# Kernel optimization log

Hardware: AMD Instinct MI355X
Metric: run time of the kernel (lower is better)

## Reference

```python
import jax, jax.numpy as jnp
import numpy as np

T = 262144  # time steps (~700 years daily)
HID = 32    # M100 hidden width


def setup_inputs() -> dict:
    key = jax.random.key(0)
    ks = jax.random.split(key, 10)
    # forward arg: inputs [T, 5] = [s_snow, s_water, precp, tmean, time]
    s_snow = jax.random.uniform(ks[0], (T,), jnp.float32) * 10.0
    s_water = jax.random.uniform(ks[1], (T,), jnp.float32) * 100.0
    precp = jax.random.uniform(ks[2], (T,), jnp.float32) * 10.0   # mm/day, >=0
    tmean = jax.random.normal(ks[3], (T,), jnp.float32) * 10.0    # deg C
    time = jnp.arange(T, dtype=jnp.float32)                       # integer day grid
    inputs = jnp.stack([s_snow, s_water, precp, tmean, time], axis=-1)
    # forward arg: day-length forcing (separate interpolator in original)
    lday = jax.random.uniform(ks[4], (T,), jnp.float32) * 0.5 + 0.2
    # M100 MLP params: 4 -> 32 -> 32 -> 5, tanh hidden
    scale = 0.2
    W1 = jax.random.normal(ks[5], (4, HID), jnp.float32) * scale
    b1 = jnp.zeros((HID,), jnp.float32)
    W2 = jax.random.normal(ks[6], (HID, HID), jnp.float32) * scale
    b2 = jnp.zeros((HID,), jnp.float32)
    W3 = jax.random.normal(ks[7], (HID, 5), jnp.float32) * scale
    b3 = jnp.zeros((5,), jnp.float32)
    return {"inputs": inputs, "lday": lday, "W1": W1, "b1": b1,
            "W2": W2, "b2": b2, "W3": W3, "b3": b3}


def reference(inputs, lday, W1, b1, W2, b2, W3, b3):
    precp = inputs[:, 2]
    tmean = inputs[:, 3]
    time = inputs[:, 4]
    n = precp.shape[0]

    def step_fn(x):
        return (jnp.tanh(5.0 * x) + 1.0) * 0.5

    def mlp(x):  # works on [4] or [N,4]
        h = jnp.tanh(x @ W1 + b1)
        h = jnp.tanh(h @ W2 + b2)
        return h @ W3 + b3

    def interp(f, t):  # periodic linear interpolation on the unit day grid
        i0 = jnp.floor(t)
        frac = t - i0
        i = jnp.mod(i0.astype(jnp.int32), n)
        ip = jnp.mod(i + 1, n)
        return f[i] * (1.0 - frac) + f[ip] * frac

    def rhs(t, y):  # hybrid_model_mlp: MLP-parameterized ExpHydro fluxes
        s0, s1 = y[0], y[1]
        p = interp(precp, t)
        tm = interp(tmean, t)
        ld = interp(lday, t)
        o = mlp(jnp.stack([s0, s1, p, tm]))
        p_snow = jax.nn.relu(jnp.sinh(o[0]) * step_fn(-tm))
        p_rain = jax.nn.relu(jnp.sinh(o[1]))
        m = jax.nn.relu(step_fn(s0) * jnp.sinh(o[2]))
        et = step_fn(s1) * jnp.exp(o[3]) * ld
        q = step_fn(s1) * jnp.exp(o[4])
        return jnp.stack([p_snow - m, p_rain + m - et - q])

    y0 = jnp.stack([inputs[0, 0], inputs[0, 1]])  # [2]
    t0s = time[:-1]
    dts = time[1:] - time[:-1]

    def scan_step(y, tdt):  # classic RK4 step between saved time points
        t, dt = tdt
        k1 = rhs(t, y)
        k2 = rhs(t + 0.5 * dt, y + 0.5 * dt * k1)
        k3 = rhs(t + 0.5 * dt, y + 0.5 * dt * k2)
        k4 = rhs(t + dt, y + dt * k3)
        yn = y + (dt / 6.0) * (k1 + 2.0 * k2 + 2.0 * k3 + k4)
        return yn, yn

    _, ys = jax.lax.scan(scan_step, y0, (t0s, dts))
    ys = jnp.concatenate([y0[None, :], ys], axis=0)  # [T, 2]

    s_snow_nn = jnp.maximum(ys[:, 0], 0.0)
    s_water_nn = jnp.maximum(ys[:, 1], 0.0)
    inputs_nn = jnp.stack([s_snow_nn, s_water_nn, precp, tmean], axis=-1)  # [T, 4]
    out = mlp(inputs_nn)  # [T, 5]
    return out[:, -1]      # q head
```

## Files before the change

### kernel.cpp

```cpp
#include <hip/hip_runtime.h>
#include <math.h>

#define T_TOTAL 262144
#define HID 32
#define WIN 2048
#define WLEN (T_TOTAL / WIN)
#define NSWEEP 6
#define FD_EPS0 4.0
#define FD_EPS1 8.0
#define LOG2E 1.4426950408889634f
#define TANH2C 2.8853900817779268f
#define NEG10LOG2E (-14.426950408889634f)
#define POS10LOG2E (14.426950408889634f)

#define PIN(x) asm volatile("" : "+v"(x))

typedef _Float16 f16x8 __attribute__((ext_vector_type(8)));
typedef float f32x4 __attribute__((ext_vector_type(4)));

__device__ __forceinline__ float fexp2(float x) { return __builtin_amdgcn_exp2f(x); }
__device__ __forceinline__ float frcp(float x)  { return __builtin_amdgcn_rcpf(x); }
__device__ __forceinline__ float fast_sig10(float x) {
    return frcp(1.0f + fexp2(x * NEG10LOG2E));
}
__device__ __forceinline__ float fast_tanh_clamp(float x) {
    float xc = __builtin_amdgcn_fmed3f(x, -9.0f, 9.0f);
    float u  = fexp2(xc * TANH2C);
    return fmaf(-2.0f, frcp(u + 1.0f), 1.0f);
}
__device__ __forceinline__ float fast_tanh_nc(float x) {
    float u = fexp2(x * TANH2C);
    return fmaf(-2.0f, frcp(u + 1.0f), 1.0f);
}

template <int CTRL>
__device__ __forceinline__ float dpp_add(float v) {
    int t = __builtin_amdgcn_update_dpp(0, __float_as_int(v), CTRL, 0xF, 0xF, true);
    return v + __int_as_float(t);
}
__device__ __forceinline__ float allsum16(float x) {
    x = dpp_add<0xB1>(x);
    x = dpp_add<0x4E>(x);
    x = dpp_add<0x141>(x);
    x = dpp_add<0x140>(x);
    return x;
}
__device__ __forceinline__ int dpp_xor1_i(int v) {
    return __builtin_amdgcn_update_dpp(0, v, 0xB1, 0xF, 0xF, true);
}
__device__ __forceinline__ float rl(float x, int lane) {
    return __int_as_float(__builtin_amdgcn_readlane(__float_as_int(x), lane));
}
__device__ __forceinline__ float bpf(int addr, float x) {
    return __int_as_float(__builtin_amdgcn_ds_bpermute(addr, __float_as_int(x)));
}

__global__ void init_kernel(const float* __restrict__ inputs, float2* icg) {
    int w = blockIdx.x * blockDim.x + threadIdx.x;
    if (w < WIN) icg[w] = make_float2(inputs[0], inputs[1]);
}

__global__ __launch_bounds__(64, 1) void sweep_kernel(
    const float* __restrict__ inputs,
    const float* __restrict__ lday,
    const float* __restrict__ W1, const float* __restrict__ b1,
    const float* __restrict__ W2, const float* __restrict__ b2,
    const float* __restrict__ W3, const float* __restrict__ b3,
    float* __restrict__ traj,
    const float2* __restrict__ icg,
    double2* __restrict__ E)
{
    const int lane = threadIdx.x;
    const int col  = lane & 15;
    const int quad = lane >> 4;
    const int j32  = lane & 31;
    const int half = lane >> 5;
    const bool odd = (lane & 1) != 0;

    const int wnd  = blockIdx.x;
    const int S    = wnd * WLEN;
    const int endStep = (S + WLEN < T_TOTAL - 1) ? (S + WLEN) : (T_TOTAL - 1);

    float w1c0 = W1[0 * HID + j32] * TANH2C, w1c1 = W1[1 * HID + j32] * TANH2C;
    float w1c2 = W1[2 * HID + j32] * TANH2C, w1c3 = W1[3 * HID + j32] * TANH2C;
    float b1j = b1[j32] * TANH2C;
    PIN(w1c0); PIN(w1c1); PIN(w1c2); PIN(w1c3); PIN(b1j);

    f16x8 Bhi0, Blo0, Bhi1, Blo1;
#pragma unroll
    for (int jj = 0; jj < 8; ++jj) {
        float w0 = W2[(quad * 8 + jj) * HID + col] * TANH2C;
        float w1v = W2[(quad * 8 + jj) * HID + col + 16] * TANH2C;
        _Float16 h0 = (_Float16)w0, h1v = (_Float16)w1v;
        Bhi0[jj] = h0;  Blo0[jj] = (_Float16)(w0 - (float)h0);
        Bhi1[jj] = h1v; Blo1[jj] = (_Float16)(w1v - (float)h1v);
    }
    PIN(Bhi0); PIN(Blo0); PIN(Bhi1); PIN(Blo1);

    float b2a2 = b2[col] * TANH2C, b2b2 = b2[col + 16] * TANH2C;
    f32x4 cb0 = {b2a2, b2a2, b2a2, b2a2};
    f32x4 cb1 = {b2b2, b2b2, b2b2, b2b2};
    PIN(cb0); PIN(cb1);

    float wca[5], wcb[5];
#pragma unroll
    for (int c = 0; c < 5; ++c) {
        wca[c] = W3[col * 5 + c] * LOG2E;
        wcb[c] = W3[(col + 16) * 5 + c] * LOG2E;
        PIN(wca[c]); PIN(wcb[c]);
    }

    float m0 = (col == 0) ? 1.f : 0.f;
    float m1 = (col == 1) ? 1.f : 0.f;
    float m2 = (col == 2) ? 1.f : 0.f;
    float m3 = (col == 3) ? 1.f : 0.f;
    float m4 = (col == 4) ? 1.f : 0.f;
    float m5 = (col == 5) ? 1.f : 0.f;
    float m6 = (col == 6) ? 1.f : 0.f;
    float m7 = (col == 7) ? 1.f : 0.f;
    float m8 = (col == 8) ? 1.f : 0.f;
    float sig1m = (col >= 5 && col <= 8) ? 1.f : 0.f;
    float zb = b3[(col < 5) ? col : 0];
    float zconst = (col < 5) ? zb * LOG2E : 0.f;
    PIN(m0); PIN(m1); PIN(m2); PIN(m3); PIN(m4); PIN(m5); PIN(m6); PIN(m7); PIN(m8);
    PIN(sig1m); PIN(zconst);

    int psel = (lane & 1) ? 0x01000504 : 0x05040100;
    int l3 = lane & 3;
    int roff = (l3 == 1) ? 128 : (l3 == 2) ? 4 : (l3 == 3) ? 132 : 0;
    int bbase = 32 * quad + roff;
    int bp0 = bbase, bp1 = bbase + 8, bp2 = bbase + 16, bp3 = bbase + 24;
    PIN(psel); PIN(bp0); PIN(bp1); PIN(bp2); PIN(bp3);

    int qb = 64 * quad;
    int a_sh0 = qb + 0,  a_sh1 = qb + 4,  a_sh2 = qb + 8;
    int a_e3  = qb + 12, a_e4  = qb + 16, a_sg0 = qb + 20, a_sg1 = qb + 24;
    PIN(a_sh0); PIN(a_sh1); PIN(a_sh2); PIN(a_e3); PIN(a_e4); PIN(a_sg0); PIN(a_sg1);

    float2 ic = icg[wnd];
    double y0 = (double)ic.x + ((quad == 1) ? FD_EPS0 : 0.0);
    double y1 = (double)ic.y + ((quad >= 2) ? FD_EPS1 : 0.0);
    float2* traj2 = (float2*)traj;
    if (lane == 0 && wnd == 0)
        traj2[0] = make_float2(ic.x, ic.y);

    auto rhs = [&](float s0q, float s1q, float base, float stm, float ld, float zoffk,
                   float& d0, float& d1, float& rout) {
        float s0A = rl(s0q, 0),  s1A = rl(s1q, 0);
        float s0B = rl(s0q, 16), s1B = rl(s1q, 16);
        float s0C = rl(s0q, 32), s1C = rl(s1q, 32);
        float s0p = half ? s0B : s0A;
        float s1p = half ? s1B : s1A;
        float prep = fmaf(s1p, w1c1, fmaf(s0p, w1c0, base));
        float prec = fmaf(s1C, w1c1, fmaf(s0C, w1c0, base));
        float up_ = fexp2(prep);
        float uc_ = fexp2(prec);
        float h1p = fmaf(-2.0f, frcp(up_ + 1.0f), 1.0f);
        float h1c = fmaf(-2.0f, frcp(uc_ + 1.0f), 1.0f);
        union { _Float16 h; unsigned short u; } cvp, cvc;
        cvp.h = (_Float16)h1p; cvc.h = (_Float16)h1c;
        int ownp = (int)cvp.u, ownc = (int)cvc.u;
        int nbp = dpp_xor1_i(ownp), nbc = dpp_xor1_i(ownc);
        int pkp = __builtin_amdgcn_perm(nbp, ownp, psel);
        int pkc = __builtin_amdgcn_perm(nbc, ownc, psel);
        int pk  = odd ? pkc : pkp;
        int g0i = __builtin_amdgcn_ds_bpermute(bp0, pk);
        int g1i = __builtin_amdgcn_ds_bpermute(bp1, pk);
        int g2i = __builtin_amdgcn_ds_bpermute(bp2, pk);
        int g3i = __builtin_amdgcn_ds_bpermute(bp3, pk);
        union { int i[4]; f16x8 h; } au;
        au.i[0] = g0i; au.i[1] = g1i; au.i[2] = g2i; au.i[3] = g3i;
        f16x8 A = au.h;
        f32x4 zz = {0.f, 0.f, 0.f, 0.f};
        f32x4 chi0 = __builtin_amdgcn_mfma_f32_16x16x32_f16(A, Bhi0, cb0, 0, 0, 0);
        f32x4 clo0 = __builtin_amdgcn_mfma_f32_16x16x32_f16(A, Blo0, zz, 0, 0, 0);
        f32x4 chi1 = __builtin_amdgcn_mfma_f32_16x16x32_f16(A, Bhi1, cb1, 0, 0, 0);
        f32x4 clo1 = __builtin_amdgcn_mfma_f32_16x16x32_f16(A, Blo1, zz, 0, 0, 0);
        float tA0 = chi0[0] + clo0[0], tB0 = chi0[1] + clo0[1], tC0 = chi0[2] + clo0[2];
        float tA1 = chi1[0] + clo1[0], tB1 = chi1[1] + clo1[1], tC1 = chi1[2] + clo1[2];
        float t0 = (quad == 1) ? tB0 : (quad >= 2) ? tC0 : tA0;
        float t1 = (quad == 1) ? tB1 : (quad >= 2) ? tC1 : tA1;
        float ua = fexp2(t0);
        float ub = fexp2(t1);
        float g0 = fmaf(-2.0f, frcp(ua + 1.0f), 1.0f);
        float g1 = fmaf(-2.0f, frcp(ub + 1.0f), 1.0f);
        float r0 = fmaf(g0, wca[0], g1 * wcb[0]);
        float r1 = fmaf(g0, wca[1], g1 * wcb[1]);
        float r2 = fmaf(g0, wca[2], g1 * wcb[2]);
        float r3 = fmaf(g0, wca[3], g1 * wcb[3]);
        float r4 = fmaf(g0, wca[4], g1 * wcb[4]);
        float s0r = allsum16(r0);
        float s1r = allsum16(r1);
        float s2r = allsum16(r2);
        float s3r = allsum16(r3);
        float s4r = allsum16(r4);
        float zs0 = s0q * NEG10LOG2E;
        float zs1 = s1q * NEG10LOG2E;
        float zoff = fmaf(zs0, m5, fmaf(zs1, m6, zoffk));
        float zarg = fmaf(s0r, m0, fmaf(s1r, m1, fmaf(s2r, m2,
                     fmaf(s3r, m3, fmaf(s4r, m4, zoff)))));
        float u = fexp2(zarg);
        float r = frcp(u + sig1m);
        float w = fmaf(0.5f, u, -0.5f * r);
        float sh0 = bpf(a_sh0, w), sh1 = bpf(a_sh1, w), sh2 = bpf(a_sh2, w);
        float e3  = bpf(a_e3, u),  e4  = bpf(a_e4, u);
        float sg0 = bpf(a_sg0, r), sg1 = bpf(a_sg1, r);
        float p_snow = fmaxf(sh0 * stm, 0.f);
        float p_rain = fmaxf(sh1, 0.f);
        float melt   = fmaxf(sg0 * sh2, 0.f);
        float etq    = sg1 * fmaf(e3, ld, e4);
        d0 = p_snow - melt;
        d1 = (p_rain + melt) - etq;
        rout = r;
    };

    float pA = inputs[S * 5 + 2],       tmA = inputs[S * 5 + 3],       ldA = lday[S];
    float pB = inputs[(S + 1) * 5 + 2], tmB = inputs[(S + 1) * 5 + 3], ldB = lday[S + 1];
    float pC = inputs[(S + 2) * 5 + 2], tmC = inputs[(S + 2) * 5 + 3], ldC = lday[S + 2];
    float stmA = fast_sig10(-tmA);
    float stmB = fast_sig10(-tmB);
    float stmm = fast_sig10(-0.5f * (tmA + tmB));
    float baseA = fmaf(pA, w1c2, fmaf(tmA, w1c3, b1j));
    float baseB = fmaf(pB, w1c2, fmaf(tmB, w1c3, b1j));

    for (int n = S; n < endStep; ++n) {
        const float ldm = 0.5f * (ldA + ldB);
        const float pm  = 0.5f * (pA + pB);
        const float tmm = 0.5f * (tmA + tmB);
        const float basem = fmaf(pm, w1c2, fmaf(tmm, w1c3, b1j));
        const float ztm_m = (0.5f * (tmB + tmC)) * POS10LOG2E;
        const float ztm_b = tmC * POS10LOG2E;
        const float zoffk = fmaf(ztm_m, m7, fmaf(ztm_b, m8, zconst));

        const float fy0 = (float)y0, fy1 = (float)y1;
        float k10, k11, k20, k21, k30, k31, k40, k41, rd;
        rhs(fy0,                  fy1,                  baseA, stmA, ldA, zoffk, k10, k11, rd);
        rhs(fmaf(0.5f, k10, fy0), fmaf(0.5f, k11, fy1), basem, stmm, ldm, zoffk, k20, k21, rd);
        rhs(fmaf(0.5f, k20, fy0), fmaf(0.5f, k21, fy1), basem, stmm, ldm, zoffk, k30, k31, rd);
        rhs(fy0 + k30,            fy1 + k31,            baseB, stmB, ldB, zoffk, k40, k41, rd);
        const float stmm_n = rl(rd, 7);
        const float stmB_n = rl(rd, 8);

        const float s0sum = (k10 + 2.0f * k20) + (2.0f * k30 + k40);
        const float s1sum = (k11 + 2.0f * k21) + (2.0f * k31 + k41);
        y0 += (1.0 / 6.0) * (double)s0sum;
        y1 += (1.0 / 6.0) * (double)s1sum;

        if (lane == 0)
            traj2[n + 1] = make_float2((float)y0, (float)y1);

        stmA = stmB; stmB = stmB_n; stmm = stmm_n;
        baseA = baseB;
        baseB = fmaf(pC, w1c2, fmaf(tmC, w1c3, b1j));
        pA = pB; tmA = tmB; ldA = ldB;
        pB = pC; tmB = tmC; ldB = ldC;
        const int np3 = (n + 3 < T_TOTAL) ? (n + 3) : (T_TOTAL - 1);
        pC = inputs[np3 * 5 + 2]; tmC = inputs[np3 * 5 + 3]; ldC = lday[np3];
    }

    if (lane == 0)  E[wnd]           = make_double2(y0, y1);
    if (lane == 16) E[WIN + wnd]     = make_double2(y0, y1);
    if (lane == 32) E[2 * WIN + wnd] = make_double2(y0, y1);
}

__global__ __launch_bounds__(64) void correct_kernel(
    const float* __restrict__ inputs,
    const double2* __restrict__ E,
    float2* __restrict__ icg) {
    __shared__ float sJ00[WIN], sJ10[WIN], sJ11[WIN];
    __shared__ float sE0x[WIN], sE0y[WIN];
    __shared__ float sGx[WIN], sGy[WIN];
    for (int i = threadIdx.x; i < WIN; i += 64) {
        double2 e0 = E[i];
        double2 e1 = E[WIN + i];
        double2 e2 = E[2 * WIN + i];
        float2 g   = icg[i];
        float J00 = (float)((e1.x - e0.x) * (1.0 / FD_EPS0));
        float J10 = (float)((e1.y - e0.y) * (1.0 / FD_EPS0));
        float J11 = (float)((e2.y - e0.y) * (1.0 / FD_EPS1));
        sJ00[i] = fminf(fmaxf(J00, -0.15f), 1.15f);
        sJ10[i] = fminf(fmaxf(J10, -0.30f), 1.80f);
        sJ11[i] = fminf(fmaxf(J11,  0.00f), 1.10f);
        sE0x[i] = (float)e0.x; sE0y[i] = (float)e0.y;
        sGx[i]  = g.x;         sGy[i]  = g.y;
    }
    __syncthreads();
    if (threadIdx.x != 0) return;

    float y0c = inputs[0];
    float y1c = inputs[1];
#pragma unroll 8
    for (int w = 0; w < WIN; ++w) {
        float d0 = y0c - sGx[w];
        float d1 = y1c - sGy[w];
        d0 = fminf(fmaxf(d0, -50.0f), 50.0f);
        d1 = fminf(fmaxf(d1, -400.0f), 400.0f);
        icg[w] = make_float2(y0c, y1c);
        y0c = fmaf(sJ00[w], d0, sE0x[w]);
        y1c = fmaf(sJ10[w], d0, fmaf(sJ11[w], d1, sE0y[w]));
        y0c = fminf(fmaxf(y0c, -5.0f), 1000.0f);
        y1c = fminf(fmaxf(y1c, -5.0f), 5000.0f);
    }
}

__global__ __launch_bounds__(256) void out_kernel(
    const float* __restrict__ inputs,
    const float* __restrict__ traj,
    const float* __restrict__ W1, const float* __restrict__ b1,
    const float* __restrict__ W2, const float* __restrict__ b2,
    const float* __restrict__ W3, const float* __restrict__ b3,
    float* __restrict__ out)
{
    __shared__ float sW1[4 * HID];
    __shared__ float sb1[HID];
    __shared__ float sW2T[HID * HID];
    __shared__ float sb2[HID];
    __shared__ float sw3[HID];
    for (int i = threadIdx.x; i < 4 * HID; i += 256) sW1[i] = W1[i];
    for (int i = threadIdx.x; i < HID; i += 256) {
        sb1[i] = b1[i]; sb2[i] = b2[i]; sw3[i] = W3[i * 5 + 4];
    }
    for (int idx = threadIdx.x; idx < HID * HID; idx += 256) {
        int jj = idx >> 5, ii = idx & 31;
        sW2T[idx] = W2[ii * HID + jj];
    }
    __syncthreads();

    int t = blockIdx.x * 256 + threadIdx.x;
    if (t >= T_TOTAL) return;

    float2 st = ((const float2*)traj)[t];
    float s0 = fmaxf(st.x, 0.0f);
    float s1 = fmaxf(st.y, 0.0f);
    float p  = inputs[t * 5 + 2];
    float tm = inputs[t * 5 + 3];

    float h1[HID];
#pragma unroll
    for (int jj = 0; jj < HID; ++jj) {
        float pre = fmaf(s0, sW1[jj], fmaf(s1, sW1[HID + jj],
                    fmaf(p, sW1[2 * HID + jj],
                    fmaf(tm, sW1[3 * HID + jj], sb1[jj]))));
        h1[jj] = fast_tanh_clamp(pre);
    }
    float o = b3[4];
#pragma unroll 4
    for (int jj = 0; jj < HID; ++jj) {
        float a0 = sb2[jj], a1 = 0.f, a2 = 0.f, a3 = 0.f;
#pragma unroll
        for (int ii = 0; ii < HID; ii += 4) {
            a0 = fmaf(h1[ii + 0], sW2T[jj * HID + ii + 0], a0);
            a1 = fmaf(h1[ii + 1], sW2T[jj * HID + ii + 1], a1);
            a2 = fmaf(h1[ii + 2], sW2T[jj * HID + ii + 2], a2);
            a3 = fmaf(h1[ii + 3], sW2T[jj * HID + ii + 3], a3);
        }
        o = fmaf(fast_tanh_nc((a0 + a1) + (a2 + a3)), sw3[jj], o);
    }
    out[t] = o;
}

extern "C" void kernel_launch(void* const* d_in, const int* in_sizes, int n_in,
                              void* d_out, int out_size, void* d_ws, size_t ws_size,
                              hipStream_t stream) {
    (void)in_sizes; (void)n_in; (void)out_size; (void)ws_size;
    const float* inputs = (const float*)d_in[0];
    const float* lday   = (const float*)d_in[1];
    const float* W1     = (const float*)d_in[2];
    const float* b1     = (const float*)d_in[3];
    const float* W2     = (const float*)d_in[4];
    const float* b2     = (const float*)d_in[5];
    const float* W3     = (const float*)d_in[6];
    const float* b3     = (const float*)d_in[7];
    float* out  = (float*)d_out;
    float* traj = (float*)d_ws;

    char* scr = (char*)d_out;
    double2* E  = (double2*)scr;
    float2* icg = (float2*)(scr + 131072);

    hipLaunchKernelGGL(init_kernel, dim3((WIN + 255) / 256), dim3(256), 0, stream,
                       inputs, icg);
    for (int k = 0; k < NSWEEP - 1; ++k) {
        hipLaunchKernelGGL(sweep_kernel, dim3(WIN), dim3(64), 0, stream,
                           inputs, lday, W1, b1, W2, b2, W3, b3, traj, icg, E);
        hipLaunchKernelGGL(correct_kernel, dim3(1), dim3(64), 0, stream,
                           inputs, E, icg);
    }
    hipLaunchKernelGGL(sweep_kernel, dim3(WIN), dim3(64), 0, stream,
                       inputs, lday, W1, b1, W2, b2, W3, b3, traj, icg, E);
    hipLaunchKernelGGL(out_kernel, dim3((T_TOTAL + 255) / 256), dim3(256), 0, stream,
                       inputs, traj, W1, b1, W2, b2, W3, b3, out);
}
```

Baseline: 2.208 ms.

## Split trajectory into 3072 uneven windows and stream guesses in correction pass

Raises the number of parallel shooting windows from 2048 to 3072, using uneven window lengths of 85 or 86 steps so that 262144 steps divide across them. This shortens the serial RK4 chain each sweep block must walk and adds more blocks to fill the GPU. The correction kernel no longer stages the previous guesses in shared memory; it reads them from global memory eight at a time, prefetching the next group while processing the current one. The serial correction loop grows by half, shorter windows may change how well the Newton-like correction converges within the fixed sweep count, and the scratch offsets in the output buffer are moved to fit the larger arrays.

```diff
diff --git a/kernel.cpp b/kernel.cpp
--- a/kernel.cpp
+++ b/kernel.cpp
@@ -3,8 +3,7 @@
 
 #define T_TOTAL 262144
 #define HID 32
-#define WIN 2048
-#define WLEN (T_TOTAL / WIN)
+#define WIN 3072
 #define NSWEEP 6
 #define FD_EPS0 4.0
 #define FD_EPS1 8.0
@@ -78,8 +77,9 @@
     const bool odd = (lane & 1) != 0;
 
     const int wnd  = blockIdx.x;
-    const int S    = wnd * WLEN;
-    const int endStep = (S + WLEN < T_TOTAL - 1) ? (S + WLEN) : (T_TOTAL - 1);
+    const int S    = wnd * 85 + ((wnd < 1024) ? wnd : 1024);
+    const int LEN  = (wnd < 1024) ? 86 : 85;
+    const int endStep = (S + LEN < T_TOTAL - 1) ? (S + LEN) : (T_TOTAL - 1);
 
     float w1c0 = W1[0 * HID + j32] * TANH2C, w1c1 = W1[1 * HID + j32] * TANH2C;
     float w1c2 = W1[2 * HID + j32] * TANH2C, w1c3 = W1[3 * HID + j32] * TANH2C;
@@ -269,12 +269,10 @@
     float2* __restrict__ icg) {
     __shared__ float sJ00[WIN], sJ10[WIN], sJ11[WIN];
     __shared__ float sE0x[WIN], sE0y[WIN];
-    __shared__ float sGx[WIN], sGy[WIN];
     for (int i = threadIdx.x; i < WIN; i += 64) {
         double2 e0 = E[i];
         double2 e1 = E[WIN + i];
         double2 e2 = E[2 * WIN + i];
-        float2 g   = icg[i];
         float J00 = (float)((e1.x - e0.x) * (1.0 / FD_EPS0));
         float J10 = (float)((e1.y - e0.y) * (1.0 / FD_EPS0));
         float J11 = (float)((e2.y - e0.y) * (1.0 / FD_EPS1));
@@ -282,25 +280,42 @@
         sJ10[i] = fminf(fmaxf(J10, -0.30f), 1.80f);
         sJ11[i] = fminf(fmaxf(J11,  0.00f), 1.10f);
         sE0x[i] = (float)e0.x; sE0y[i] = (float)e0.y;
-        sGx[i]  = g.x;         sGy[i]  = g.y;
     }
     __syncthreads();
     if (threadIdx.x != 0) return;
 
     float y0c = inputs[0];
     float y1c = inputs[1];
-#pragma unroll 8
-    for (int w = 0; w < WIN; ++w) {
-        float d0 = y0c - sGx[w];
-        float d1 = y1c - sGy[w];
-        d0 = fminf(fmaxf(d0, -50.0f), 50.0f);
-        d1 = fminf(fmaxf(d1, -400.0f), 400.0f);
-        icg[w] = make_float2(y0c, y1c);
-        y0c = fmaf(sJ00[w], d0, sE0x[w]);
-        y1c = fmaf(sJ10[w], d0, fmaf(sJ11[w], d1, sE0y[w]));
-        y0c = fminf(fmaxf(y0c, -5.0f), 1000.0f);
-        y1c = fminf(fmaxf(y1c, -5.0f), 5000.0f);
-    }
+
+#define PROC(G, W)                                              \
+    {                                                           \
+        float d0 = y0c - (G).x;                                 \
+        float d1 = y1c - (G).y;                                 \
+        d0 = fminf(fmaxf(d0, -50.0f), 50.0f);                   \
+        d1 = fminf(fmaxf(d1, -400.0f), 400.0f);                 \
+        icg[W] = make_float2(y0c, y1c);                         \
+        y0c = fmaf(sJ00[W], d0, sE0x[W]);                       \
+        y1c = fmaf(sJ10[W], d0, fmaf(sJ11[W], d1, sE0y[W]));    \
+        y0c = fminf(fmaxf(y0c, -5.0f), 1000.0f);                \
+        y1c = fminf(fmaxf(y1c, -5.0f), 5000.0f);                \
+    }
+
+    float2 g0 = icg[0], g1 = icg[1], g2 = icg[2], g3 = icg[3];
+    float2 g4 = icg[4], g5 = icg[5], g6 = icg[6], g7 = icg[7];
+    for (int base = 0; base < WIN; base += 8) {
+        int nb = base + 8;
+        float2 t0, t1, t2, t3, t4, t5, t6, t7;
+        if (nb < WIN) {
+            t0 = icg[nb + 0]; t1 = icg[nb + 1]; t2 = icg[nb + 2]; t3 = icg[nb + 3];
+            t4 = icg[nb + 4]; t5 = icg[nb + 5]; t6 = icg[nb + 6]; t7 = icg[nb + 7];
+        } else {
+            t0 = g0; t1 = g1; t2 = g2; t3 = g3; t4 = g4; t5 = g5; t6 = g6; t7 = g7;
+        }
+        PROC(g0, base + 0); PROC(g1, base + 1); PROC(g2, base + 2); PROC(g3, base + 3);
+        PROC(g4, base + 4); PROC(g5, base + 5); PROC(g6, base + 6); PROC(g7, base + 7);
+        g0 = t0; g1 = t1; g2 = t2; g3 = t3; g4 = t4; g5 = t5; g6 = t6; g7 = t7;
+    }
+#undef PROC
 }
 
 __global__ __launch_bounds__(256) void out_kernel(
@@ -376,7 +391,7 @@
 
     char* scr = (char*)d_out;
     double2* E  = (double2*)scr;
-    float2* icg = (float2*)(scr + 131072);
+    float2* icg = (float2*)(scr + 196608);
 
     hipLaunchKernelGGL(init_kernel, dim3((WIN + 255) / 256), dim3(256), 0, stream,
                        inputs, icg);
```

Result: slower. 2.379 ms (+7.8%).

## Split trajectory into more shorter windows and double-buffer the correction staging

Applied to the files above, without the earlier changes.

Raises the window count from 2048 to 3072 and spreads steps unevenly (86 or 85 per window), so each sweep block runs a shorter serial RK4 chain. The correction kernel now stages window data in double-buffered chunks of 1024, letting the other 63 threads load the next chunk while thread 0 runs the serial correction recurrence. This cuts the per-sweep critical path, but the serial correction pass gets longer, more blocks compete for CUs, and the scratch offsets grow. More windows may also slow convergence of the fixed six-sweep scheme and hurt accuracy.

```diff
diff --git a/kernel.cpp b/kernel.cpp
--- a/kernel.cpp
+++ b/kernel.cpp
@@ -3,9 +3,9 @@
 
 #define T_TOTAL 262144
 #define HID 32
-#define WIN 2048
-#define WLEN (T_TOTAL / WIN)
+#define WIN 3072
 #define NSWEEP 6
+#define CH 1024
 #define FD_EPS0 4.0
 #define FD_EPS1 8.0
 #define LOG2E 1.4426950408889634f
@@ -78,8 +78,9 @@
     const bool odd = (lane & 1) != 0;
 
     const int wnd  = blockIdx.x;
-    const int S    = wnd * WLEN;
-    const int endStep = (S + WLEN < T_TOTAL - 1) ? (S + WLEN) : (T_TOTAL - 1);
+    const int S    = wnd * 85 + ((wnd < 1024) ? wnd : 1024);
+    const int LEN  = (wnd < 1024) ? 86 : 85;
+    const int endStep = (S + LEN < T_TOTAL - 1) ? (S + LEN) : (T_TOTAL - 1);
 
     float w1c0 = W1[0 * HID + j32] * TANH2C, w1c1 = W1[1 * HID + j32] * TANH2C;
     float w1c2 = W1[2 * HID + j32] * TANH2C, w1c3 = W1[3 * HID + j32] * TANH2C;
@@ -267,39 +268,51 @@
     const float* __restrict__ inputs,
     const double2* __restrict__ E,
     float2* __restrict__ icg) {
-    __shared__ float sJ00[WIN], sJ10[WIN], sJ11[WIN];
-    __shared__ float sE0x[WIN], sE0y[WIN];
-    __shared__ float sGx[WIN], sGy[WIN];
-    for (int i = threadIdx.x; i < WIN; i += 64) {
-        double2 e0 = E[i];
-        double2 e1 = E[WIN + i];
-        double2 e2 = E[2 * WIN + i];
-        float2 g   = icg[i];
+    __shared__ float sJ00[2][CH], sJ10[2][CH], sJ11[2][CH];
+    __shared__ float sE0x[2][CH], sE0y[2][CH];
+    __shared__ float sGx[2][CH],  sGy[2][CH];
+    const int tid = threadIdx.x;
+
+    auto stage_one = [&](int buf, int i, int w) {
+        double2 e0 = E[w];
+        double2 e1 = E[WIN + w];
+        double2 e2 = E[2 * WIN + w];
+        float2 g   = icg[w];
         float J00 = (float)((e1.x - e0.x) * (1.0 / FD_EPS0));
         float J10 = (float)((e1.y - e0.y) * (1.0 / FD_EPS0));
         float J11 = (float)((e2.y - e0.y) * (1.0 / FD_EPS1));
-        sJ00[i] = fminf(fmaxf(J00, -0.15f), 1.15f);
-        sJ10[i] = fminf(fmaxf(J10, -0.30f), 1.80f);
-        sJ11[i] = fminf(fmaxf(J11,  0.00f), 1.10f);
-        sE0x[i] = (float)e0.x; sE0y[i] = (float)e0.y;
-        sGx[i]  = g.x;         sGy[i]  = g.y;
-    }
+        sJ00[buf][i] = fminf(fmaxf(J00, -0.15f), 1.15f);
+        sJ10[buf][i] = fminf(fmaxf(J10, -0.30f), 1.80f);
+        sJ11[buf][i] = fminf(fmaxf(J11,  0.00f), 1.10f);
+        sE0x[buf][i] = (float)e0.x; sE0y[buf][i] = (float)e0.y;
+        sGx[buf][i]  = g.x;         sGy[buf][i]  = g.y;
+    };
+
+    for (int i = tid; i < CH; i += 64) stage_one(0, i, i);
     __syncthreads();
-    if (threadIdx.x != 0) return;
 
     float y0c = inputs[0];
     float y1c = inputs[1];
-#pragma unroll 8
-    for (int w = 0; w < WIN; ++w) {
-        float d0 = y0c - sGx[w];
-        float d1 = y1c - sGy[w];
-        d0 = fminf(fmaxf(d0, -50.0f), 50.0f);
-        d1 = fminf(fmaxf(d1, -400.0f), 400.0f);
-        icg[w] = make_float2(y0c, y1c);
-        y0c = fmaf(sJ00[w], d0, sE0x[w]);
-        y1c = fmaf(sJ10[w], d0, fmaf(sJ11[w], d1, sE0y[w]));
-        y0c = fminf(fmaxf(y0c, -5.0f), 1000.0f);
-        y1c = fminf(fmaxf(y1c, -5.0f), 5000.0f);
+    for (int c = 0; c < 3; ++c) {
+        const int buf = c & 1;
+        if (tid == 0) {
+            const int wbase = c * CH;
+            for (int i = 0; i < CH; ++i) {
+                float d0 = y0c - sGx[buf][i];
+                float d1 = y1c - sGy[buf][i];
+                d0 = fminf(fmaxf(d0, -50.0f), 50.0f);
+                d1 = fminf(fmaxf(d1, -400.0f), 400.0f);
+                icg[wbase + i] = make_float2(y0c, y1c);
+                y0c = fmaf(sJ00[buf][i], d0, sE0x[buf][i]);
+                y1c = fmaf(sJ10[buf][i], d0, fmaf(sJ11[buf][i], d1, sE0y[buf][i]));
+                y0c = fminf(fmaxf(y0c, -5.0f), 1000.0f);
+                y1c = fminf(fmaxf(y1c, -5.0f), 5000.0f);
+            }
+        } else if (c + 1 < 3) {
+            for (int i = tid - 1; i < CH; i += 63)
+                stage_one((c + 1) & 1, i, (c + 1) * CH + i);
+        }
+        __syncthreads();
     }
 }
 
@@ -376,7 +389,7 @@
 
     char* scr = (char*)d_out;
     double2* E  = (double2*)scr;
-    float2* icg = (float2*)(scr + 131072);
+    float2* icg = (float2*)(scr + 196608);
 
     hipLaunchKernelGGL(init_kernel, dim3((WIN + 255) / 256), dim3(256), 0, stream,
                        inputs, icg);
```

After: 2.526 ms. +14.4%, slower.
